# Kernel optimization log

Measured on AMD Instinct MI355X. Metric: run time of the kernel, lower is better.

The kernel has to match this reference:

```python
import jax, jax.numpy as jnp
import numpy as np

B = 8192
H = 1024            # hidden_size
A = 512             # alphabet_size
S = 2               # sequence_length
D_IN = A * S        # 1024, gate input dim
D1, D2 = H // 2, H // 3   # decoder dims: 512, 341
TEMP = 1.0


def _linear_params(key, out_d, in_d):
    kw, kb = jax.random.split(key)
    lim = 1.0 / np.sqrt(in_d)
    W = jax.random.uniform(kw, (out_d, in_d), minval=-lim, maxval=lim, dtype=jnp.float32)
    b = jax.random.uniform(kb, (out_d,), minval=-lim, maxval=lim, dtype=jnp.float32)
    return W, b


def setup_inputs() -> dict:
    key = jax.random.key(0)
    ks = jax.random.split(key, 16)
    inp = {
        'x': jax.random.normal(ks[0], (B, D_IN), dtype=jnp.float32),
        'h': jax.random.normal(ks[1], (B, H), dtype=jnp.float32),
        'c': jax.random.normal(ks[2], (B, H), dtype=jnp.float32),
    }
    names = [('W_fi', 'b_fi', H, D_IN), ('W_fh', 'b_fh', H, H),
             ('W_ii', 'b_ii', H, D_IN), ('W_ih', 'b_ih', H, H),
             ('W_si', 'b_si', H, D_IN), ('W_sh', 'b_sh', H, H),
             ('W_oi', 'b_oi', H, D_IN), ('W_oh', 'b_oh', H, H),
             ('W_d1', 'b_d1', D1, H), ('W_d2', 'b_d2', D2, D1),
             ('W_d3', 'b_d3', A, D2)]
    for k, (wn, bn, od, idm) in zip(ks[3:3 + len(names)], names):
        W, b = _linear_params(k, od, idm)
        inp[wn] = W
        inp[bn] = b
    return inp


def reference(x, h, c,
              W_fi, b_fi, W_fh, b_fh,
              W_ii, b_ii, W_ih, b_ih,
              W_si, b_si, W_sh, b_sh,
              W_oi, b_oi, W_oh, b_oh,
              W_d1, b_d1, W_d2, b_d2, W_d3, b_d3):
    def lin(v, W, b):
        return v @ W.T + b

    f = jax.nn.sigmoid(lin(x, W_fi, b_fi) + lin(h, W_fh, b_fh))
    i = jax.nn.sigmoid(lin(x, W_ii, b_ii) + lin(h, W_ih, b_ih))
    s = jnp.tanh(lin(x, W_si, b_si) + lin(h, W_sh, b_sh))
    o = jax.nn.sigmoid(lin(x, W_oi, b_oi) + lin(h, W_oh, b_oh))
    c_new = c * f + i * s
    h_new = o * jnp.tanh(c_new)
    d = jnp.tanh(lin(h_new, W_d1, b_d1))
    d = jnp.tanh(lin(d, W_d2, b_d2))
    d = jax.nn.softmax(lin(d, W_d3, b_d3) / TEMP, axis=-1)
    return h_new, d
```

## Files before the change

kernel.cpp:

```cpp
#include <hip/hip_runtime.h>
#include <cstdint>
#include <cstddef>


typedef _Float16 half_t;
typedef _Float16 half8 __attribute__((ext_vector_type(8)));
typedef _Float16 half4v __attribute__((ext_vector_type(4)));
typedef float float4v __attribute__((ext_vector_type(4)));

#define GLD_LDS16(gptr, lptr)                                                  \
  __builtin_amdgcn_global_load_lds(                                            \
      (const __attribute__((address_space(1))) void*)(gptr),                   \
      (__attribute__((address_space(3))) void*)(lptr), 16, 0, 0)

__device__ __forceinline__ float fsig(float x) {
  return 1.0f / (1.0f + __expf(-x));
}
__device__ __forceinline__ float ftanh_(float x) {
  const float e = __expf(2.0f * x);
  return 1.0f - 2.0f / (e + 1.0f);
}

__global__ __launch_bounds__(256) void gemm_gates(const half_t* __restrict__ A,
                                                  const half_t* __restrict__ Bw,
                                                  const float* __restrict__ bias,
                                                  const float* __restrict__ cin,
                                                  float* __restrict__ hout,
                                                  half_t* __restrict__ h2) {
  constexpr int K = 2048;
  __shared__ alignas(16) half_t As[128 * 32];
  __shared__ alignas(16) half_t Bs[128 * 32];
  const int tid = threadIdx.x;
  const int lane = tid & 63;
  const int wave = tid >> 6;
  const int m = lane & 15;
  const int q = lane >> 4;
  const int sx = (m >> 1) & 3;
  const size_t tile_m = (size_t)blockIdx.y * 128;
  const size_t tile_n = (size_t)blockIdx.x * 128;
  const int wm = (wave >> 1) * 64;
  const int wn = (wave & 1) * 64;

  const int cA0 = tid, rA0 = cA0 >> 2, kA0 = ((cA0 & 3) ^ ((rA0 >> 1) & 3));
  const int cA1 = 256 + tid, rA1 = cA1 >> 2, kA1 = ((cA1 & 3) ^ ((rA1 >> 1) & 3));
  const half_t* Ag0 = A + (tile_m + rA0) * (size_t)K + kA0 * 8;
  const half_t* Ag1 = A + (tile_m + rA1) * (size_t)K + kA1 * 8;
  const half_t* Bg0 = Bw + (tile_n + rA0) * (size_t)K + kA0 * 8;
  const half_t* Bg1 = Bw + (tile_n + rA1) * (size_t)K + kA1 * 8;
  const int p0 = cA0 * 16, p1 = cA1 * 16;

  float4v acc[4][4] = {};
  for (int k0 = 0; k0 < K; k0 += 32) {
    __syncthreads();
    GLD_LDS16(Ag0 + k0, (char*)As + p0);
    GLD_LDS16(Ag1 + k0, (char*)As + p1);
    GLD_LDS16(Bg0 + k0, (char*)Bs + p0);
    GLD_LDS16(Bg1 + k0, (char*)Bs + p1);
    __syncthreads();
    const int ks = (q ^ sx) * 8;
    half8 af[4], bf[4];
#pragma unroll
    for (int i = 0; i < 4; ++i)
      af[i] = *(const half8*)(As + (wm + i * 16 + m) * 32 + ks);
#pragma unroll
    for (int j = 0; j < 4; ++j)
      bf[j] = *(const half8*)(Bs + (wn + j * 16 + m) * 32 + ks);
#pragma unroll
    for (int i = 0; i < 4; ++i)
#pragma unroll
      for (int j = 0; j < 4; ++j)
        acc[i][j] =
            __builtin_amdgcn_mfma_f32_16x16x32_f16(af[i], bf[j], acc[i][j], 0, 0, 0);
  }

  const int nwave = (int)tile_n + wn;
  const size_t u = (size_t)((nwave >> 6) << 4) + m;
  float bg[4];
#pragma unroll
  for (int g = 0; g < 4; ++g) bg[g] = bias[nwave + g * 16 + m];
#pragma unroll
  for (int i = 0; i < 4; ++i) {
#pragma unroll
    for (int r = 0; r < 4; ++r) {
      const size_t row = tile_m + wm + q * 4 + i * 16 + r;
      const size_t off = row * 1024 + u;
      const float F = fsig(acc[i][0][r] + bg[0]);
      const float I = fsig(acc[i][1][r] + bg[1]);
      const float S = ftanh_(acc[i][2][r] + bg[2]);
      const float O = fsig(acc[i][3][r] + bg[3]);
      const float cn = cin[off] * F + I * S;
      const float hn = O * ftanh_(cn);
      hout[off] = hn;
      h2[off] = (half_t)hn;
    }
  }
}

__global__ __launch_bounds__(512) void decoder_fused(
    const half_t* __restrict__ H2,
    const half_t* __restrict__ W1,
    const float* __restrict__ b1,
    const half_t* __restrict__ W2,
    const float* __restrict__ b2,
    const half_t* __restrict__ W3,
    const float* __restrict__ b3,
    float* __restrict__ out) {
  __shared__ alignas(16) half_t Bs[512 * 32];
  __shared__ alignas(16) half_t As[16 * 40];
  __shared__ alignas(16) half_t d1s[16 * 520];
  __shared__ alignas(16) half_t d2s[16 * 392];
  __shared__ float red[8 * 16];
  __shared__ float rowred[16];

  const int tid = threadIdx.x;
  const int lane = tid & 63;
  const int w = tid >> 6;
  const int m = lane & 15;
  const int q = lane >> 4;
  const int sx = (m >> 1) & 3;
  const size_t r0 = (size_t)blockIdx.x * 16;

  {
    float4v acc[4] = {};
    for (int kk = 0; kk < 1024; kk += 32) {
      __syncthreads();
#pragma unroll
      for (int p = 0; p < 4; ++p) {
        const int cch = p * 512 + tid;
        const int n = cch >> 2;
        const int kq = (cch & 3) ^ ((n >> 1) & 3);
        GLD_LDS16(W1 + (size_t)n * 1024 + kk + kq * 8, (char*)Bs + cch * 16);
      }
      if (tid < 64) {
        const int row = tid >> 2;
        const int kq = tid & 3;
        const half8 v = *(const half8*)(H2 + (r0 + row) * 1024 + kk + kq * 8);
        *(half8*)(As + row * 40 + kq * 8) = v;
      }
      __syncthreads();
      const int ks = (q ^ sx) * 8;
      const half8 af = *(const half8*)(As + m * 40 + q * 8);
      half8 bf[4];
#pragma unroll
      for (int j = 0; j < 4; ++j)
        bf[j] = *(const half8*)(Bs + (w * 64 + j * 16 + m) * 32 + ks);
#pragma unroll
      for (int j = 0; j < 4; ++j)
        acc[j] = __builtin_amdgcn_mfma_f32_16x16x32_f16(af, bf[j], acc[j], 0, 0, 0);
    }
#pragma unroll
    for (int j = 0; j < 4; ++j) {
      const int col = w * 64 + j * 16 + m;
      const float bv = b1[col];
#pragma unroll
      for (int r = 0; r < 4; ++r)
        d1s[(q * 4 + r) * 520 + col] = (half_t)ftanh_(acc[j][r] + bv);
    }
  }

  {
    float4v acc[3] = {};
    for (int kk = 0; kk < 512; kk += 32) {
      __syncthreads();
#pragma unroll
      for (int p = 0; p < 3; ++p) {
        const int cch = p * 512 + tid;
        const int n = cch >> 2;
        const int kq = (cch & 3) ^ ((n >> 1) & 3);
        GLD_LDS16(W2 + (size_t)n * 512 + kk + kq * 8, (char*)Bs + cch * 16);
      }
      __syncthreads();
      const int ks = (q ^ sx) * 8;
      const half8 af = *(const half8*)(d1s + m * 520 + kk + q * 8);
      half8 bf[3];
#pragma unroll
      for (int j = 0; j < 3; ++j)
        bf[j] = *(const half8*)(Bs + (w * 48 + j * 16 + m) * 32 + ks);
#pragma unroll
      for (int j = 0; j < 3; ++j)
        acc[j] = __builtin_amdgcn_mfma_f32_16x16x32_f16(af, bf[j], acc[j], 0, 0, 0);
    }
#pragma unroll
    for (int j = 0; j < 3; ++j) {
      const int col = w * 48 + j * 16 + m;
      const float bv = b2[col];
#pragma unroll
      for (int r = 0; r < 4; ++r)
        d2s[(q * 4 + r) * 392 + col] = (half_t)ftanh_(acc[j][r] + bv);
    }
  }

  {
    float4v acc[4] = {};
    for (int kk = 0; kk < 384; kk += 32) {
      __syncthreads();
#pragma unroll
      for (int p = 0; p < 4; ++p) {
        const int cch = p * 512 + tid;
        const int n = cch >> 2;
        const int kq = (cch & 3) ^ ((n >> 1) & 3);
        GLD_LDS16(W3 + (size_t)n * 384 + kk + kq * 8, (char*)Bs + cch * 16);
      }
      __syncthreads();
      const int ks = (q ^ sx) * 8;
      const half8 af = *(const half8*)(d2s + m * 392 + kk + q * 8);
      half8 bf[4];
#pragma unroll
      for (int j = 0; j < 4; ++j)
        bf[j] = *(const half8*)(Bs + (w * 64 + j * 16 + m) * 32 + ks);
#pragma unroll
      for (int j = 0; j < 4; ++j)
        acc[j] = __builtin_amdgcn_mfma_f32_16x16x32_f16(af, bf[j], acc[j], 0, 0, 0);
    }
    float lg[4][4];
#pragma unroll
    for (int j = 0; j < 4; ++j) {
      const float bv = b3[w * 64 + j * 16 + m];
#pragma unroll
      for (int r = 0; r < 4; ++r) lg[j][r] = acc[j][r] + bv;
    }
    float pmax[4];
#pragma unroll
    for (int r = 0; r < 4; ++r) {
      float v = fmaxf(fmaxf(lg[0][r], lg[1][r]), fmaxf(lg[2][r], lg[3][r]));
#pragma unroll
      for (int d = 1; d < 16; d <<= 1) v = fmaxf(v, __shfl_xor(v, d, 64));
      pmax[r] = v;
    }
    if (m == 0) {
#pragma unroll
      for (int r = 0; r < 4; ++r) red[w * 16 + q * 4 + r] = pmax[r];
    }
    __syncthreads();
    if (tid < 16) {
      float v = red[tid];
#pragma unroll
      for (int ww = 1; ww < 8; ++ww) v = fmaxf(v, red[ww * 16 + tid]);
      rowred[tid] = v;
    }
    __syncthreads();
    float ex[4][4], psum[4];
#pragma unroll
    for (int r = 0; r < 4; ++r) {
      const float M = rowred[q * 4 + r];
      float s = 0.f;
#pragma unroll
      for (int j = 0; j < 4; ++j) {
        ex[j][r] = __expf(lg[j][r] - M);
        s += ex[j][r];
      }
#pragma unroll
      for (int d = 1; d < 16; d <<= 1) s += __shfl_xor(s, d, 64);
      psum[r] = s;
    }
    if (m == 0) {
#pragma unroll
      for (int r = 0; r < 4; ++r) red[w * 16 + q * 4 + r] = psum[r];
    }
    __syncthreads();
    if (tid < 16) {
      float s = 0.f;
#pragma unroll
      for (int ww = 0; ww < 8; ++ww) s += red[ww * 16 + tid];
      rowred[tid] = 1.0f / s;
    }
    __syncthreads();
#pragma unroll
    for (int r = 0; r < 4; ++r) {
      const int row = q * 4 + r;
      const float inv = rowred[row];
#pragma unroll
      for (int j = 0; j < 4; ++j)
        out[(r0 + row) * 512 + w * 64 + j * 16 + m] = ex[j][r] * inv;
    }
  }
}

__global__ void prep_pack(const float* __restrict__ x, const float* __restrict__ h,
                          const float* __restrict__ Wfi, const float* __restrict__ Wfh,
                          const float* __restrict__ Wii, const float* __restrict__ Wih,
                          const float* __restrict__ Wsi, const float* __restrict__ Wsh,
                          const float* __restrict__ Woi, const float* __restrict__ Woh,
                          half_t* __restrict__ xh, half_t* __restrict__ wall) {
  const int bid = blockIdx.x;
  const float* src;
  half_t* dst;
  size_t idx;
  if (bid < 16384) {
    idx = ((size_t)bid * 256 + threadIdx.x) * 4;
    const size_t b = idx >> 11;
    const int col = (int)(idx & 2047);
    src = (col < 1024) ? (x + b * 1024 + col) : (h + b * 1024 + (col - 1024));
    dst = xh + idx;
  } else {
    idx = ((size_t)(bid - 16384) * 256 + threadIdx.x) * 4;
    const int n = (int)(idx >> 11);
    const int col = (int)(idx & 2047);
    const int g = (n >> 4) & 3;
    const size_t u = (size_t)(((n >> 6) << 4) | (n & 15));
    const float* Wi = (g == 0) ? Wfi : (g == 1) ? Wii : (g == 2) ? Wsi : Woi;
    const float* Wh = (g == 0) ? Wfh : (g == 1) ? Wih : (g == 2) ? Wsh : Woh;
    src = (col < 1024) ? (Wi + u * 1024 + col) : (Wh + u * 1024 + (col - 1024));
    dst = wall + idx;
  }
  const float4v v = *(const float4v*)src;
  half4v o;
  o.x = (half_t)v.x; o.y = (half_t)v.y; o.z = (half_t)v.z; o.w = (half_t)v.w;
  *(half4v*)dst = o;
}

__global__ void prep_small(const float* __restrict__ Wd1, const float* __restrict__ Wd2,
                           const float* __restrict__ Wd3, const float* __restrict__ bd2,
                           const float* __restrict__ bfi, const float* __restrict__ bfh,
                           const float* __restrict__ bii, const float* __restrict__ bih,
                           const float* __restrict__ bsi, const float* __restrict__ bsh,
                           const float* __restrict__ boi, const float* __restrict__ boh,
                           half_t* __restrict__ WD1, half_t* __restrict__ WD2h,
                           half_t* __restrict__ WD3h, float* __restrict__ BALL,
                           float* __restrict__ BD2) {
  const int bid = blockIdx.x;
  const int tid = threadIdx.x;
  if (bid < 512) {
    const size_t i4 = ((size_t)bid * 256 + tid) * 4;
    const float4v v = *(const float4v*)(Wd1 + i4);
    half4v o;
    o.x = (half_t)v.x; o.y = (half_t)v.y; o.z = (half_t)v.z; o.w = (half_t)v.w;
    *(half4v*)(WD1 + i4) = o;
  } else if (bid < 704) {
    const size_t i4 = ((size_t)(bid - 512) * 256 + tid) * 4;
    const int r = (int)(i4 >> 9);
    const int cc = (int)(i4 & 511);
    half4v o;
    if (r < 341) {
      const float4v v = *(const float4v*)(Wd2 + (size_t)r * 512 + cc);
      o.x = (half_t)v.x; o.y = (half_t)v.y; o.z = (half_t)v.z; o.w = (half_t)v.w;
    } else {
      o.x = (half_t)0.f; o.y = (half_t)0.f; o.z = (half_t)0.f; o.w = (half_t)0.f;
    }
    *(half4v*)(WD2h + i4) = o;
  } else if (bid < 896) {
    const size_t i4 = ((size_t)(bid - 704) * 256 + tid) * 4;
    const int r = (int)(i4 / 384);
    const int cc = (int)(i4 - (size_t)r * 384);
    half4v o;
    o.x = (cc + 0 < 341) ? (half_t)Wd3[(size_t)r * 341 + cc + 0] : (half_t)0.f;
    o.y = (cc + 1 < 341) ? (half_t)Wd3[(size_t)r * 341 + cc + 1] : (half_t)0.f;
    o.z = (cc + 2 < 341) ? (half_t)Wd3[(size_t)r * 341 + cc + 2] : (half_t)0.f;
    o.w = (cc + 3 < 341) ? (half_t)Wd3[(size_t)r * 341 + cc + 3] : (half_t)0.f;
    *(half4v*)(WD3h + i4) = o;
  } else if (bid < 912) {
    const int n = (bid - 896) * 256 + tid;
    const int g = (n >> 4) & 3;
    const int u = ((n >> 6) << 4) | (n & 15);
    const float* bi = (g == 0) ? bfi : (g == 1) ? bii : (g == 2) ? bsi : boi;
    const float* bh = (g == 0) ? bfh : (g == 1) ? bih : (g == 2) ? bsh : boh;
    BALL[n] = bi[u] + bh[u];
  } else {
    const int i = (bid - 912) * 256 + tid;
    if (i < 384) BD2[i] = (i < 341) ? bd2[i] : 0.0f;
  }
}

extern "C" void kernel_launch(void* const* d_in, const int* in_sizes, int n_in,
                              void* d_out, int out_size, void* d_ws, size_t ws_size,
                              hipStream_t stream) {
  const float* x = (const float*)d_in[0];
  const float* h = (const float*)d_in[1];
  const float* c = (const float*)d_in[2];
  const float* Wfi = (const float*)d_in[3];  const float* bfi = (const float*)d_in[4];
  const float* Wfh = (const float*)d_in[5];  const float* bfh = (const float*)d_in[6];
  const float* Wii = (const float*)d_in[7];  const float* bii = (const float*)d_in[8];
  const float* Wih = (const float*)d_in[9];  const float* bih = (const float*)d_in[10];
  const float* Wsi = (const float*)d_in[11]; const float* bsi = (const float*)d_in[12];
  const float* Wsh = (const float*)d_in[13]; const float* bsh = (const float*)d_in[14];
  const float* Woi = (const float*)d_in[15]; const float* boi = (const float*)d_in[16];
  const float* Woh = (const float*)d_in[17]; const float* boh = (const float*)d_in[18];
  const float* Wd1 = (const float*)d_in[19]; const float* bd1 = (const float*)d_in[20];
  const float* Wd2 = (const float*)d_in[21]; const float* bd2 = (const float*)d_in[22];
  const float* Wd3 = (const float*)d_in[23]; const float* bd3 = (const float*)d_in[24];

  char* ws = (char*)d_ws;
  size_t o = 0;
  auto alloc = [&](size_t bytes) {
    size_t cur = o;
    o += (bytes + 255) & ~(size_t)255;
    return cur;
  };
  half_t* XH   = (half_t*)(ws + alloc((size_t)8192 * 2048 * 2));
  half_t* WALL = (half_t*)(ws + alloc((size_t)4096 * 2048 * 2));
  float*  BALL = (float*)(ws + alloc(4096 * 4));
  half_t* WD1  = (half_t*)(ws + alloc((size_t)512 * 1024 * 2));
  half_t* WD2  = (half_t*)(ws + alloc((size_t)384 * 512 * 2));
  float*  BD2  = (float*)(ws + alloc(384 * 4));
  half_t* WD3  = (half_t*)(ws + alloc((size_t)512 * 384 * 2));
  half_t* H2   = (half_t*)(ws + alloc((size_t)8192 * 1024 * 2));

  float* h_out = (float*)d_out;
  float* d_outp = (float*)d_out + (size_t)8192 * 1024;

  prep_pack<<<24576, 256, 0, stream>>>(x, h, Wfi, Wfh, Wii, Wih, Wsi, Wsh, Woi, Woh,
                                       XH, WALL);
  prep_small<<<914, 256, 0, stream>>>(Wd1, Wd2, Wd3, bd2, bfi, bfh, bii, bih, bsi, bsh,
                                      boi, boh, WD1, WD2, WD3, BALL, BD2);

  gemm_gates<<<dim3(32, 64), 256, 0, stream>>>(XH, WALL, BALL, c, h_out, H2);

  decoder_fused<<<512, 512, 0, stream>>>(H2, WD1, bd1, WD2, BD2, WD3, bd3, d_outp);
}
```

Before: 449.4 us.

## Drop fp16 h copy, remap gate tiles per XCD, load decoder weights directly

The gate GEMM no longer writes a separate fp16 copy of h_new. The decoder instead reads the fp32 h_out, converts it to fp16 in LDS once per block, and loads weight fragments straight from global memory into registers rather than staging them through LDS with barriers. The gate GEMM grid is flattened to 1D and remapped so each XCD works on a fixed group of N tiles, which should improve L2 reuse of the weight tiles. The decoder now uses 256 threads, each wave handling twice the columns. This drops per-iteration barriers and an 8192x1024 fp16 write, at the cost of uncoalesced, strided global weight reads in the decoder and twice as many fp32 activation bytes read.

```diff
diff --git a/kernel.cpp b/kernel.cpp
--- a/kernel.cpp
+++ b/kernel.cpp
@@ -25,8 +25,7 @@
                                                   const half_t* __restrict__ Bw,
                                                   const float* __restrict__ bias,
                                                   const float* __restrict__ cin,
-                                                  float* __restrict__ hout,
-                                                  half_t* __restrict__ h2) {
+                                                  float* __restrict__ hout) {
   constexpr int K = 2048;
   __shared__ alignas(16) half_t As[128 * 32];
   __shared__ alignas(16) half_t Bs[128 * 32];
@@ -36,8 +35,12 @@
   const int m = lane & 15;
   const int q = lane >> 4;
   const int sx = (m >> 1) & 3;
-  const size_t tile_m = (size_t)blockIdx.y * 128;
-  const size_t tile_n = (size_t)blockIdx.x * 128;
+
+  const int bid = blockIdx.x;
+  const int xcd = bid & 7;
+  const int l = bid >> 3;
+  const size_t tile_n = (size_t)((xcd << 2) | (l & 3)) * 128;
+  const size_t tile_m = (size_t)(l >> 2) * 128;
   const int wm = (wave >> 1) * 64;
   const int wn = (wave & 1) * 64;
 
@@ -91,13 +94,12 @@
       const float cn = cin[off] * F + I * S;
       const float hn = O * ftanh_(cn);
       hout[off] = hn;
-      h2[off] = (half_t)hn;
-    }
-  }
-}
-
-__global__ __launch_bounds__(512) void decoder_fused(
-    const half_t* __restrict__ H2,
+    }
+  }
+}
+
+__global__ __launch_bounds__(256) void decoder_fused(
+    const float* __restrict__ hsrc,
     const half_t* __restrict__ W1,
     const float* __restrict__ b1,
     const half_t* __restrict__ W2,
@@ -105,11 +107,10 @@
     const half_t* __restrict__ W3,
     const float* __restrict__ b3,
     float* __restrict__ out) {
-  __shared__ alignas(16) half_t Bs[512 * 32];
-  __shared__ alignas(16) half_t As[16 * 40];
+  __shared__ alignas(16) half_t As[16 * 1032];
   __shared__ alignas(16) half_t d1s[16 * 520];
   __shared__ alignas(16) half_t d2s[16 * 392];
-  __shared__ float red[8 * 16];
+  __shared__ float red[4 * 16];
   __shared__ float rowred[16];
 
   const int tid = threadIdx.x;
@@ -117,112 +118,93 @@
   const int w = tid >> 6;
   const int m = lane & 15;
   const int q = lane >> 4;
-  const int sx = (m >> 1) & 3;
   const size_t r0 = (size_t)blockIdx.x * 16;
 
+#pragma unroll
+  for (int i = 0; i < 16; ++i) {
+    const int e = (tid + i * 256) * 4;
+    const int row = e >> 10, col = e & 1023;
+    const float4v v = *(const float4v*)(hsrc + (r0 + row) * 1024 + col);
+    half4v hv;
+    hv.x = (half_t)v.x; hv.y = (half_t)v.y; hv.z = (half_t)v.z; hv.w = (half_t)v.w;
+    *(half4v*)(As + row * 1032 + col) = hv;
+  }
+  __syncthreads();
+
   {
-    float4v acc[4] = {};
+    float4v acc[8] = {};
+    const int c0 = w * 128 + m;
     for (int kk = 0; kk < 1024; kk += 32) {
-      __syncthreads();
-#pragma unroll
-      for (int p = 0; p < 4; ++p) {
-        const int cch = p * 512 + tid;
-        const int n = cch >> 2;
-        const int kq = (cch & 3) ^ ((n >> 1) & 3);
-        GLD_LDS16(W1 + (size_t)n * 1024 + kk + kq * 8, (char*)Bs + cch * 16);
-      }
-      if (tid < 64) {
-        const int row = tid >> 2;
-        const int kq = tid & 3;
-        const half8 v = *(const half8*)(H2 + (r0 + row) * 1024 + kk + kq * 8);
-        *(half8*)(As + row * 40 + kq * 8) = v;
-      }
-      __syncthreads();
-      const int ks = (q ^ sx) * 8;
-      const half8 af = *(const half8*)(As + m * 40 + q * 8);
-      half8 bf[4];
-#pragma unroll
-      for (int j = 0; j < 4; ++j)
-        bf[j] = *(const half8*)(Bs + (w * 64 + j * 16 + m) * 32 + ks);
-#pragma unroll
-      for (int j = 0; j < 4; ++j)
+      const half8 af = *(const half8*)(As + m * 1032 + kk + q * 8);
+      half8 bf[8];
+#pragma unroll
+      for (int j = 0; j < 8; ++j)
+        bf[j] = *(const half8*)(W1 + (size_t)(c0 + j * 16) * 1024 + kk + q * 8);
+#pragma unroll
+      for (int j = 0; j < 8; ++j)
         acc[j] = __builtin_amdgcn_mfma_f32_16x16x32_f16(af, bf[j], acc[j], 0, 0, 0);
     }
 #pragma unroll
-    for (int j = 0; j < 4; ++j) {
-      const int col = w * 64 + j * 16 + m;
+    for (int j = 0; j < 8; ++j) {
+      const int col = c0 + j * 16;
       const float bv = b1[col];
 #pragma unroll
       for (int r = 0; r < 4; ++r)
         d1s[(q * 4 + r) * 520 + col] = (half_t)ftanh_(acc[j][r] + bv);
     }
   }
+  __syncthreads();
 
   {
-    float4v acc[3] = {};
+    float4v acc[6] = {};
+    const int c0 = w * 96 + m;
     for (int kk = 0; kk < 512; kk += 32) {
-      __syncthreads();
-#pragma unroll
-      for (int p = 0; p < 3; ++p) {
-        const int cch = p * 512 + tid;
-        const int n = cch >> 2;
-        const int kq = (cch & 3) ^ ((n >> 1) & 3);
-        GLD_LDS16(W2 + (size_t)n * 512 + kk + kq * 8, (char*)Bs + cch * 16);
-      }
-      __syncthreads();
-      const int ks = (q ^ sx) * 8;
       const half8 af = *(const half8*)(d1s + m * 520 + kk + q * 8);
-      half8 bf[3];
-#pragma unroll
-      for (int j = 0; j < 3; ++j)
-        bf[j] = *(const half8*)(Bs + (w * 48 + j * 16 + m) * 32 + ks);
-#pragma unroll
-      for (int j = 0; j < 3; ++j)
+      half8 bf[6];
+#pragma unroll
+      for (int j = 0; j < 6; ++j)
+        bf[j] = *(const half8*)(W2 + (size_t)(c0 + j * 16) * 512 + kk + q * 8);
+#pragma unroll
+      for (int j = 0; j < 6; ++j)
         acc[j] = __builtin_amdgcn_mfma_f32_16x16x32_f16(af, bf[j], acc[j], 0, 0, 0);
     }
 #pragma unroll
-    for (int j = 0; j < 3; ++j) {
-      const int col = w * 48 + j * 16 + m;
+    for (int j = 0; j < 6; ++j) {
+      const int col = c0 + j * 16;
       const float bv = b2[col];
 #pragma unroll
       for (int r = 0; r < 4; ++r)
         d2s[(q * 4 + r) * 392 + col] = (half_t)ftanh_(acc[j][r] + bv);
     }
   }
+  __syncthreads();
 
   {
-    float4v acc[4] = {};
+    float4v acc[8] = {};
+    const int c0 = w * 128 + m;
     for (int kk = 0; kk < 384; kk += 32) {
-      __syncthreads();
-#pragma unroll
-      for (int p = 0; p < 4; ++p) {
-        const int cch = p * 512 + tid;
-        const int n = cch >> 2;
-        const int kq = (cch & 3) ^ ((n >> 1) & 3);
-        GLD_LDS16(W3 + (size_t)n * 384 + kk + kq * 8, (char*)Bs + cch * 16);
-      }
-      __syncthreads();
-      const int ks = (q ^ sx) * 8;
       const half8 af = *(const half8*)(d2s + m * 392 + kk + q * 8);
-      half8 bf[4];
-#pragma unroll
-      for (int j = 0; j < 4; ++j)
-        bf[j] = *(const half8*)(Bs + (w * 64 + j * 16 + m) * 32 + ks);
-#pragma unroll
-      for (int j = 0; j < 4; ++j)
+      half8 bf[8];
+#pragma unroll
+      for (int j = 0; j < 8; ++j)
+        bf[j] = *(const half8*)(W3 + (size_t)(c0 + j * 16) * 384 + kk + q * 8);
+#pragma unroll
+      for (int j = 0; j < 8; ++j)
         acc[j] = __builtin_amdgcn_mfma_f32_16x16x32_f16(af, bf[j], acc[j], 0, 0, 0);
     }
-    float lg[4][4];
-#pragma unroll
-    for (int j = 0; j < 4; ++j) {
-      const float bv = b3[w * 64 + j * 16 + m];
+    float lg[8][4];
+#pragma unroll
+    for (int j = 0; j < 8; ++j) {
+      const float bv = b3[c0 + j * 16];
 #pragma unroll
       for (int r = 0; r < 4; ++r) lg[j][r] = acc[j][r] + bv;
     }
     float pmax[4];
 #pragma unroll
     for (int r = 0; r < 4; ++r) {
-      float v = fmaxf(fmaxf(lg[0][r], lg[1][r]), fmaxf(lg[2][r], lg[3][r]));
+      float v = lg[0][r];
+#pragma unroll
+      for (int j = 1; j < 8; ++j) v = fmaxf(v, lg[j][r]);
 #pragma unroll
       for (int d = 1; d < 16; d <<= 1) v = fmaxf(v, __shfl_xor(v, d, 64));
       pmax[r] = v;
@@ -235,17 +217,17 @@
     if (tid < 16) {
       float v = red[tid];
 #pragma unroll
-      for (int ww = 1; ww < 8; ++ww) v = fmaxf(v, red[ww * 16 + tid]);
+      for (int ww = 1; ww < 4; ++ww) v = fmaxf(v, red[ww * 16 + tid]);
       rowred[tid] = v;
     }
     __syncthreads();
-    float ex[4][4], psum[4];
+    float ex[8][4], psum[4];
 #pragma unroll
     for (int r = 0; r < 4; ++r) {
       const float M = rowred[q * 4 + r];
       float s = 0.f;
 #pragma unroll
-      for (int j = 0; j < 4; ++j) {
+      for (int j = 0; j < 8; ++j) {
         ex[j][r] = __expf(lg[j][r] - M);
         s += ex[j][r];
       }
@@ -261,7 +243,7 @@
     if (tid < 16) {
       float s = 0.f;
 #pragma unroll
-      for (int ww = 0; ww < 8; ++ww) s += red[ww * 16 + tid];
+      for (int ww = 0; ww < 4; ++ww) s += red[ww * 16 + tid];
       rowred[tid] = 1.0f / s;
     }
     __syncthreads();
@@ -270,8 +252,8 @@
       const int row = q * 4 + r;
       const float inv = rowred[row];
 #pragma unroll
-      for (int j = 0; j < 4; ++j)
-        out[(r0 + row) * 512 + w * 64 + j * 16 + m] = ex[j][r] * inv;
+      for (int j = 0; j < 8; ++j)
+        out[(r0 + row) * 512 + c0 + j * 16] = ex[j][r] * inv;
     }
   }
 }
@@ -393,7 +375,6 @@
   half_t* WD2  = (half_t*)(ws + alloc((size_t)384 * 512 * 2));
   float*  BD2  = (float*)(ws + alloc(384 * 4));
   half_t* WD3  = (half_t*)(ws + alloc((size_t)512 * 384 * 2));
-  half_t* H2   = (half_t*)(ws + alloc((size_t)8192 * 1024 * 2));
 
   float* h_out = (float*)d_out;
   float* d_outp = (float*)d_out + (size_t)8192 * 1024;
@@ -403,7 +384,7 @@
   prep_small<<<914, 256, 0, stream>>>(Wd1, Wd2, Wd3, bd2, bfi, bfh, bii, bih, bsi, bsh,
                                       boi, boh, WD1, WD2, WD3, BALL, BD2);
 
-  gemm_gates<<<dim3(32, 64), 256, 0, stream>>>(XH, WALL, BALL, c, h_out, H2);
-
-  decoder_fused<<<512, 512, 0, stream>>>(H2, WD1, bd1, WD2, BD2, WD3, bd3, d_outp);
-}
+  gemm_gates<<<2048, 256, 0, stream>>>(XH, WALL, BALL, c, h_out);
+
+  decoder_fused<<<512, 256, 0, stream>>>(h_out, WD1, bd1, WD2, BD2, WD3, bd3, d_outp);
+}
```

After: 487.9 us. 8.6% more time.
